# Kernel tuning notes

Measured on AMD Instinct MI355X. Metric: run time of the kernel, lower is better.

## Reference

```python
import math
import jax, jax.numpy as jnp
import numpy as np

HEADS = 16


def setup_inputs() -> dict:
    key = jax.random.key(0)
    k1, k2, k3, k4, k5 = jax.random.split(key, 5)
    B, S, D = 2, 2048, 1024
    return {
        "x": jax.random.normal(k1, (B, S, D), dtype=jnp.float32),
        "Wqkv": jax.random.normal(k2, (3 * D, D), dtype=jnp.float32) * (1.0 / math.sqrt(D)),
        "bqkv": jax.random.normal(k3, (3 * D,), dtype=jnp.float32) * 0.02,
        "Wo": jax.random.normal(k4, (D, D), dtype=jnp.float32) * (1.0 / math.sqrt(D)),
        "bo": jax.random.normal(k5, (D,), dtype=jnp.float32) * 0.02,
    }


def reference(x, Wqkv, bqkv, Wo, bo):
    B, S, D = x.shape
    H = HEADS
    hd = D // H  # head dim
    qkv = x @ Wqkv.T + bqkv                      # (B, S, 3D)
    # Faithful to torch: direct contiguous reshape (NOT a transpose-based head split)
    qkv = qkv.reshape(B, H, S, 3 * hd)           # (B, H, S, 3*hd)
    q, k, v = jnp.split(qkv, 3, axis=-1)         # each (B, H, S, hd)
    scores = jnp.einsum("bhsd,bhtd->bhst", q, k) * (1.0 / math.sqrt(hd))
    attn = jax.nn.softmax(scores, axis=-1)       # (B, H, S, S)
    vals = jnp.einsum("bhst,bhtd->bhsd", attn, v)
    vals = vals.reshape(B, S, D)                 # faithful direct reshape back
    return vals @ Wo.T + bo
```

## Files before the change

kernel.cpp:

```cpp
#include <hip/hip_runtime.h>
#include <stdint.h>

typedef unsigned short u16;
typedef __attribute__((ext_vector_type(8))) short short8;
typedef __attribute__((ext_vector_type(4))) float f32x4;
typedef __attribute__((ext_vector_type(16))) float f32x16;
typedef __attribute__((ext_vector_type(8))) __bf16 bf16x8;
typedef __attribute__((ext_vector_type(4))) unsigned u32x4;

#define DEV static __device__ __forceinline__

template <typename T>
DEV auto mfma_try(T a, T b, f32x4 c, int)
    -> decltype(__builtin_amdgcn_mfma_f32_16x16x32_bf16(a, b, c, 0, 0, 0)) {
  return __builtin_amdgcn_mfma_f32_16x16x32_bf16(a, b, c, 0, 0, 0);
}
template <typename T>
DEV f32x4 mfma_try(T a, T b, f32x4 c, long) {
  return __builtin_amdgcn_mfma_f32_16x16x32_bf16(
      __builtin_bit_cast(bf16x8, a), __builtin_bit_cast(bf16x8, b), c, 0, 0, 0);
}
DEV f32x4 MFMA(short8 a, short8 b, f32x4 c) { return mfma_try(a, b, c, 0); }

template <typename T>
DEV auto mfma32_try(T a, T b, f32x16 c, int)
    -> decltype(__builtin_amdgcn_mfma_f32_32x32x16_bf16(a, b, c, 0, 0, 0)) {
  return __builtin_amdgcn_mfma_f32_32x32x16_bf16(a, b, c, 0, 0, 0);
}
template <typename T>
DEV f32x16 mfma32_try(T a, T b, f32x16 c, long) {
  return __builtin_amdgcn_mfma_f32_32x32x16_bf16(
      __builtin_bit_cast(bf16x8, a), __builtin_bit_cast(bf16x8, b), c, 0, 0, 0);
}
DEV f32x16 MFMA32(short8 a, short8 b, f32x16 c) { return mfma32_try(a, b, c, 0); }

DEV void gload16(const u16* g, u16* lds) {
  __builtin_amdgcn_global_load_lds((unsigned int*)g, (unsigned int*)lds, 16, 0, 0);
}

DEV u16 f2bf(float f) {
  unsigned u = __float_as_uint(f);
  u = (u + 0x7FFFu + ((u >> 16) & 1u)) >> 16;
  return (u16)u;
}

DEV float exp2fast(float x) {
  float r;
  asm("v_exp_f32 %0, %1" : "=v"(r) : "v"(x));
  return r;
}

DEV unsigned cvtpk_bf16(float lo, float hi_) {
  unsigned r;
  asm("v_cvt_pk_bf16_f32 %0, %1, %2" : "=v"(r) : "v"(lo), "v"(hi_));
  return r;
}

DEV void permswap(unsigned& a, unsigned& b) {
  asm volatile("v_permlane32_swap_b32 %0, %1" : "+v"(a), "+v"(b));
}

__global__ void cvt_kernel(const float* __restrict__ x, const float* __restrict__ wq,
                           const float* __restrict__ wo, u16* __restrict__ xb,
                           u16* __restrict__ wqb, u16* __restrict__ wob) {
  const int N1 = 4194304 / 4, N2 = 3145728 / 4, N3 = 1048576 / 4;
  const int total = N1 + N2 + N3;
  for (int i = blockIdx.x * blockDim.x + threadIdx.x; i < total;
       i += gridDim.x * blockDim.x) {
    const float4* s;
    u16* d;
    int off;
    if (i < N1) { s = (const float4*)x; d = xb; off = i; }
    else if (i < N1 + N2) { s = (const float4*)wq; d = wqb; off = i - N1; }
    else { s = (const float4*)wo; d = wob; off = i - N1 - N2; }
    float4 v = s[off];
    ushort4 o;
    o.x = f2bf(v.x); o.y = f2bf(v.y); o.z = f2bf(v.z); o.w = f2bf(v.w);
    ((ushort4*)d)[off] = o;
  }
}

__global__ __launch_bounds__(256, 4) void gemm1_128(
    const u16* __restrict__ A, const u16* __restrict__ Bm,
    const float* __restrict__ bias,
    u16* __restrict__ Qb, u16* __restrict__ Kb, u16* __restrict__ Vb) {
  __shared__ u16 SM[128 * 136];
  u16* const As = SM;
  u16* const Bs = SM + 4096;
  const int K = 1024;
  const int tid = threadIdx.x;
  const int lane = tid & 63;
  const int wave = tid >> 6;
  const int wr = wave >> 1, wc = wave & 1;
  const int l15 = lane & 15, l4 = lane >> 4;
  const int m0 = blockIdx.y * 128, n0 = blockIdx.x * 128;

  f32x4 acc[4][4] = {};

  const u16* ga = A + (size_t)(m0 + (tid >> 2)) * K + (tid & 3) * 8;
  const u16* gb = Bm + (size_t)(n0 + (tid >> 2)) * K + (tid & 3) * 8;
  u16* la = As + tid * 8;
  u16* lb = Bs + tid * 8;
  const size_t rstep = (size_t)64 * K;

  for (int kt = 0; kt < K; kt += 32) {
    gload16(ga + kt, la);
    gload16(ga + kt + rstep, la + 2048);
    gload16(gb + kt, lb);
    gload16(gb + kt + rstep, lb + 2048);
    __syncthreads();
    short8 af[4], bfr[4];
#pragma unroll
    for (int i = 0; i < 4; ++i)
      af[i] = *(const short8*)(As + (wr * 64 + i * 16 + l15) * 32 + l4 * 8);
#pragma unroll
    for (int i = 0; i < 4; ++i)
      bfr[i] = *(const short8*)(Bs + (wc * 64 + i * 16 + l15) * 32 + l4 * 8);
#pragma unroll
    for (int i = 0; i < 4; ++i)
#pragma unroll
      for (int j = 0; j < 4; ++j) acc[i][j] = MFMA(af[i], bfr[j], acc[i][j]);
    __syncthreads();
  }

#pragma unroll
  for (int nj = 0; nj < 4; ++nj) {
    const int cl = wc * 64 + nj * 16 + l15;
    const float bv = bias[n0 + cl];
#pragma unroll
    for (int mi = 0; mi < 4; ++mi)
#pragma unroll
      for (int r = 0; r < 4; ++r) {
        const int ml = wr * 64 + mi * 16 + l4 * 4 + r;
        SM[ml * 136 + cl] = f2bf(acc[mi][nj][r] + bv);
      }
  }
  __syncthreads();

  const int ml = tid >> 1;
  const int h = tid & 1;
  const int m = m0 + ml;
  const int c0 = n0 + h * 64;
  const int chunk = c0 / 192;
  const int sel = (c0 - chunk * 192) >> 6;
  u16* const dst = (sel == 0) ? Qb : ((sel == 1) ? Kb : Vb);
  const int s = m & 2047;
  const int bh = (m >> 11) * 16 + (s >> 7);
  const int s2 = (s & 127) * 16 + chunk;
  u16* const drow = dst + ((size_t)bh * 2048 + s2) * 64;
  const u16* const srow = SM + ml * 136 + h * 64;
#pragma unroll
  for (int g = 0; g < 8; ++g)
    *(short8*)(drow + g * 8) = *(const short8*)(srow + g * 8);
}

__global__ __launch_bounds__(256, 4) void gemm2_64(
    const u16* __restrict__ A, const u16* __restrict__ Bm,
    const float* __restrict__ bias, float* __restrict__ Cf) {
  __shared__ u16 As[64 * 32];
  __shared__ u16 Bs[128 * 32];
  const int K = 1024, N = 1024;
  const int tid = threadIdx.x;
  const int lane = tid & 63;
  const int wave = tid >> 6;
  const int l15 = lane & 15, l4 = lane >> 4;
  const int m0 = blockIdx.y * 64, n0 = blockIdx.x * 128;

  f32x4 acc[4][2] = {};

  const u16* ga = A + (size_t)(m0 + (tid >> 2)) * K + (tid & 3) * 8;
  const u16* gb = Bm + (size_t)(n0 + (tid >> 2)) * K + (tid & 3) * 8;
  u16* la = As + tid * 8;
  u16* lb = Bs + tid * 8;
  const size_t rstep = (size_t)64 * K;

  for (int kt = 0; kt < K; kt += 32) {
    gload16(ga + kt, la);
    gload16(gb + kt, lb);
    gload16(gb + kt + rstep, lb + 2048);
    __syncthreads();
    short8 af[4], bfr[2];
#pragma unroll
    for (int i = 0; i < 4; ++i)
      af[i] = *(const short8*)(As + (i * 16 + l15) * 32 + l4 * 8);
#pragma unroll
    for (int j = 0; j < 2; ++j)
      bfr[j] = *(const short8*)(Bs + (wave * 32 + j * 16 + l15) * 32 + l4 * 8);
#pragma unroll
    for (int i = 0; i < 4; ++i)
#pragma unroll
      for (int j = 0; j < 2; ++j) acc[i][j] = MFMA(af[i], bfr[j], acc[i][j]);
    __syncthreads();
  }

#pragma unroll
  for (int nj = 0; nj < 2; ++nj) {
    const int c = n0 + wave * 32 + nj * 16 + l15;
    const float bv = bias[c];
#pragma unroll
    for (int mi = 0; mi < 4; ++mi)
#pragma unroll
      for (int r = 0; r < 4; ++r) {
        const int m = m0 + mi * 16 + l4 * 4 + r;
        Cf[(size_t)m * N + c] = acc[mi][nj][r] + bv;
      }
  }
}

__global__ __launch_bounds__(256) void vtrans_kernel(const u16* __restrict__ Vn,
                                                     u16* __restrict__ VT) {
  __shared__ u16 T[64 * 72];
  const int tid = threadIdx.x;
  const int bh = blockIdx.x >> 5;
  const int s0 = (blockIdx.x & 31) * 64;
  const int r = tid >> 3, c8 = tid & 7;
#pragma unroll
  for (int i = 0; i < 2; ++i) {
    const int s = r + i * 32;
    short8 v = *(const short8*)(Vn + ((size_t)bh * 2048 + s0 + s) * 64 + c8 * 8);
#pragma unroll
    for (int j = 0; j < 8; ++j) T[(c8 * 8 + j) * 72 + s] = (u16)v[j];
  }
  __syncthreads();
#pragma unroll
  for (int i = 0; i < 2; ++i) {
    const int d = (tid >> 3) + i * 32;
    short8 v = *(const short8*)(&T[d * 72 + (tid & 7) * 8]);
    *(short8*)(VT + ((size_t)bh * 64 + d) * 2048 + s0 + (tid & 7) * 8) = v;
  }
}

__global__ __launch_bounds__(512) void attn_kernel(
    const u16* __restrict__ Qg, const u16* __restrict__ Kg,
    const u16* __restrict__ VTg, u16* __restrict__ v2) {
  __shared__ __align__(16) char smem[65536];
  u16* const KS = (u16*)smem;
  u16* const VS = (u16*)smem + 16384;
  float* const FM = (float*)smem;

  const int tid = threadIdx.x;
  const int lane = tid & 63;
  const int half = tid >> 8;
  const int tid256 = tid & 255;
  const int w4 = (tid >> 6) & 3;
  const int l31 = lane & 31;
  const int hi = lane >> 5;

  const int bid = blockIdx.x;
  const int logical = (bid & 7) * 64 + (bid >> 3);
  const int bh = logical >> 4;
  const int qt = logical & 15;

  const u16* Qh = Qg + (size_t)bh * 2048 * 64;
  const u16* Kh = Kg + (size_t)bh * 2048 * 64;
  const u16* VTh = VTg + (size_t)bh * 64 * 2048;

  const int q0 = qt * 128 + w4 * 32;
  const float C1 = 0.18033688f;

  short8 qf[4];
#pragma unroll
  for (int d_ = 0; d_ < 4; ++d_)
    qf[d_] = *(const short8*)(Qh + (size_t)(q0 + l31) * 64 + d_ * 16 + hi * 8);

  f32x16 ot[2] = {};
  float ls4[4] = {0.f, 0.f, 0.f, 0.f};

  const int r8 = tid256 >> 3;
  const int c16 = tid256 & 7;
  const int xr = l31 & 7;
  const int Tbase = half * 16;

  auto stage = [&](int buf, int T) {
    u16* kd = KS + (half * 2 + buf) * 4096 + tid256 * 8;
    u16* vd = VS + (half * 2 + buf) * 4096 + tid256 * 8;
#pragma unroll
    for (int i = 0; i < 2; ++i) {
      const int row = i * 32 + r8;
      gload16(Kh + (size_t)(T * 64 + row) * 64 + ((c16 ^ (row & 7)) * 8),
              kd + i * 2048);
    }
#pragma unroll
    for (int i = 0; i < 2; ++i) {
      const int d = i * 32 + r8;
      gload16(VTh + (size_t)d * 2048 + T * 64 + ((c16 ^ (d & 7)) * 8),
              vd + i * 2048);
    }
  };

  stage(0, Tbase);
  __syncthreads();

  for (int t = 0; t < 16; ++t) {
    const int cur = t & 1;
    if (t + 1 < 16) stage(cur ^ 1, Tbase + t + 1);

    const u16* Kb = KS + (half * 2 + cur) * 4096;
    const u16* Vb = VS + (half * 2 + cur) * 4096;

    f32x16 st[2] = {};
    __builtin_amdgcn_s_setprio(1);
#pragma unroll
    for (int n = 0; n < 2; ++n)
#pragma unroll
      for (int d_ = 0; d_ < 4; ++d_) {
        short8 kf = *(const short8*)(Kb + (n * 32 + l31) * 64 +
                                     (((d_ * 2 + hi) ^ xr) * 8));
        st[n] = MFMA32(kf, qf[d_], st[n]);
      }
    __builtin_amdgcn_s_setprio(0);

#pragma unroll
    for (int r = 0; r < 16; ++r) {
      st[0][r] = exp2fast(st[0][r] * C1);
      st[1][r] = exp2fast(st[1][r] * C1);
    }
#pragma unroll
    for (int i = 0; i < 4; ++i)
      ls4[i] += ((st[0][i] + st[0][i + 4]) + (st[0][i + 8] + st[0][i + 12])) +
                ((st[1][i] + st[1][i + 4]) + (st[1][i + 8] + st[1][i + 12]));

    short8 pf[2][2];
#pragma unroll
    for (int n = 0; n < 2; ++n) {
      unsigned W[4][2];
#pragma unroll
      for (int j = 0; j < 4; ++j)
#pragma unroll
        for (int pp = 0; pp < 2; ++pp)
          W[j][pp] = cvtpk_bf16(st[n][4 * j + 2 * pp], st[n][4 * j + 2 * pp + 1]);
#pragma unroll
      for (int ks = 0; ks < 2; ++ks) {
        unsigned x0 = W[2 * ks][0], y0 = W[2 * ks + 1][0];
        unsigned x1 = W[2 * ks][1], y1 = W[2 * ks + 1][1];
        permswap(x0, y0);
        permswap(x1, y1);
        u32x4 pw = {x0, x1, y0, y1};
        pf[n][ks] = __builtin_bit_cast(short8, pw);
      }
    }

    __builtin_amdgcn_s_setprio(1);
#pragma unroll
    for (int db = 0; db < 2; ++db)
#pragma unroll
      for (int ksg = 0; ksg < 4; ++ksg) {
        short8 vf = *(const short8*)(Vb + (db * 32 + l31) * 64 +
                                     (((ksg * 2 + hi) ^ xr) * 8));
        ot[db] = MFMA32(vf, pf[ksg >> 1][ksg & 1], ot[db]);
      }
    __builtin_amdgcn_s_setprio(0);

    __syncthreads();
  }

  float l = (ls4[0] + ls4[1]) + (ls4[2] + ls4[3]);
  l += __shfl_xor(l, 32);

  if (half == 1) {
    float* F = FM + (size_t)(w4 * 64 + lane) * 33;
#pragma unroll
    for (int r = 0; r < 16; ++r) {
      F[r] = ot[0][r];
      F[16 + r] = ot[1][r];
    }
    F[32] = l;
  }
  __syncthreads();
  if (half == 0) {
    const float* F = FM + (size_t)(w4 * 64 + lane) * 33;
    const float inv = 1.0f / (l + F[32]);

    const int s2v = q0 + l31;
    const int rowO = (bh >> 4) * 2048 + (bh & 15) * 128 + (s2v >> 4);
    const int colb = (s2v & 15) * 64;
#pragma unroll
    for (int db = 0; db < 2; ++db)
#pragma unroll
      for (int g = 0; g < 4; ++g) {
        ushort4 w;
        w.x = f2bf((ot[db][4 * g + 0] + F[db * 16 + 4 * g + 0]) * inv);
        w.y = f2bf((ot[db][4 * g + 1] + F[db * 16 + 4 * g + 1]) * inv);
        w.z = f2bf((ot[db][4 * g + 2] + F[db * 16 + 4 * g + 2]) * inv);
        w.w = f2bf((ot[db][4 * g + 3] + F[db * 16 + 4 * g + 3]) * inv);
        const int d = db * 32 + 8 * g + 4 * hi;
        *(ushort4*)(v2 + (size_t)rowO * 1024 + colb + d) = w;
      }
  }
}

extern "C" void kernel_launch(void* const* d_in, const int* in_sizes, int n_in,
                              void* d_out, int out_size, void* d_ws, size_t ws_size,
                              hipStream_t stream) {
  const float* x = (const float*)d_in[0];
  const float* Wqkv = (const float*)d_in[1];
  const float* bqkv = (const float*)d_in[2];
  const float* Wo = (const float*)d_in[3];
  const float* bo = (const float*)d_in[4];
  float* out = (float*)d_out;

  char* ws = (char*)d_ws;
  u16* xb   = (u16*)(ws);
  u16* wqb  = (u16*)(ws + 8388608);
  u16* wob  = (u16*)(ws + 14680064);
  u16* Qb   = (u16*)(ws + 16777216);
  u16* Kb   = (u16*)(ws + 25165824);
  u16* VTb  = (u16*)(ws + 33554432);
  u16* v2   = (u16*)(ws + 41943040);
  u16* Vnat = v2;

  cvt_kernel<<<2048, 256, 0, stream>>>(x, Wqkv, Wo, xb, wqb, wob);

  dim3 g1(24, 32);
  gemm1_128<<<g1, 256, 0, stream>>>(xb, wqb, bqkv, Qb, Kb, Vnat);

  vtrans_kernel<<<1024, 256, 0, stream>>>(Vnat, VTb);

  attn_kernel<<<512, 512, 0, stream>>>(Qb, Kb, VTb, v2);

  dim3 g2(8, 64);
  gemm2_64<<<g2, 256, 0, stream>>>(v2, wob, bo, out);
}
```

Baseline: 118.8 us.

## Double-buffer LDS tiles in both projection GEMMs with async prefetch

```diff
diff --git a/kernel.cpp b/kernel.cpp
--- a/kernel.cpp
+++ b/kernel.cpp
@@ -85,8 +85,6 @@
     const float* __restrict__ bias,
     u16* __restrict__ Qb, u16* __restrict__ Kb, u16* __restrict__ Vb) {
   __shared__ u16 SM[128 * 136];
-  u16* const As = SM;
-  u16* const Bs = SM + 4096;
   const int K = 1024;
   const int tid = threadIdx.x;
   const int lane = tid & 63;
@@ -99,16 +97,30 @@
 
   const u16* ga = A + (size_t)(m0 + (tid >> 2)) * K + (tid & 3) * 8;
   const u16* gb = Bm + (size_t)(n0 + (tid >> 2)) * K + (tid & 3) * 8;
-  u16* la = As + tid * 8;
-  u16* lb = Bs + tid * 8;
   const size_t rstep = (size_t)64 * K;
 
-  for (int kt = 0; kt < K; kt += 32) {
+  auto stage = [&](int buf, int kt) {
+    u16* la = SM + buf * 8192 + tid * 8;
+    u16* lb = la + 4096;
     gload16(ga + kt, la);
     gload16(ga + kt + rstep, la + 2048);
     gload16(gb + kt, lb);
     gload16(gb + kt + rstep, lb + 2048);
-    __syncthreads();
+  };
+
+  stage(0, 0);
+  for (int t = 0; t < 32; ++t) {
+    const int cur = t & 1;
+    if (t + 1 < 32) {
+      stage(cur ^ 1, (t + 1) * 32);
+      asm volatile("s_waitcnt vmcnt(4)" ::: "memory");
+    } else {
+      asm volatile("s_waitcnt vmcnt(0)" ::: "memory");
+    }
+    __builtin_amdgcn_s_barrier();
+
+    const u16* As = SM + cur * 8192;
+    const u16* Bs = As + 4096;
     short8 af[4], bfr[4];
 #pragma unroll
     for (int i = 0; i < 4; ++i)
@@ -116,11 +128,13 @@
 #pragma unroll
     for (int i = 0; i < 4; ++i)
       bfr[i] = *(const short8*)(Bs + (wc * 64 + i * 16 + l15) * 32 + l4 * 8);
+    __builtin_amdgcn_s_setprio(1);
 #pragma unroll
     for (int i = 0; i < 4; ++i)
 #pragma unroll
       for (int j = 0; j < 4; ++j) acc[i][j] = MFMA(af[i], bfr[j], acc[i][j]);
-    __syncthreads();
+    __builtin_amdgcn_s_setprio(0);
+    __builtin_amdgcn_s_barrier();
   }
 
 #pragma unroll
@@ -157,8 +171,7 @@
 __global__ __launch_bounds__(256, 4) void gemm2_64(
     const u16* __restrict__ A, const u16* __restrict__ Bm,
     const float* __restrict__ bias, float* __restrict__ Cf) {
-  __shared__ u16 As[64 * 32];
-  __shared__ u16 Bs[128 * 32];
+  __shared__ u16 SM2[2 * 6144];
   const int K = 1024, N = 1024;
   const int tid = threadIdx.x;
   const int lane = tid & 63;
@@ -170,15 +183,29 @@
 
   const u16* ga = A + (size_t)(m0 + (tid >> 2)) * K + (tid & 3) * 8;
   const u16* gb = Bm + (size_t)(n0 + (tid >> 2)) * K + (tid & 3) * 8;
-  u16* la = As + tid * 8;
-  u16* lb = Bs + tid * 8;
   const size_t rstep = (size_t)64 * K;
 
-  for (int kt = 0; kt < K; kt += 32) {
+  auto stage = [&](int buf, int kt) {
+    u16* la = SM2 + buf * 6144 + tid * 8;
+    u16* lb = SM2 + buf * 6144 + 2048 + tid * 8;
     gload16(ga + kt, la);
     gload16(gb + kt, lb);
     gload16(gb + kt + rstep, lb + 2048);
-    __syncthreads();
+  };
+
+  stage(0, 0);
+  for (int t = 0; t < 32; ++t) {
+    const int cur = t & 1;
+    if (t + 1 < 32) {
+      stage(cur ^ 1, (t + 1) * 32);
+      asm volatile("s_waitcnt vmcnt(3)" ::: "memory");
+    } else {
+      asm volatile("s_waitcnt vmcnt(0)" ::: "memory");
+    }
+    __builtin_amdgcn_s_barrier();
+
+    const u16* As = SM2 + cur * 6144;
+    const u16* Bs = As + 2048;
     short8 af[4], bfr[2];
 #pragma unroll
     for (int i = 0; i < 4; ++i)
@@ -186,11 +213,13 @@
 #pragma unroll
     for (int j = 0; j < 2; ++j)
       bfr[j] = *(const short8*)(Bs + (wave * 32 + j * 16 + l15) * 32 + l4 * 8);
+    __builtin_amdgcn_s_setprio(1);
 #pragma unroll
     for (int i = 0; i < 4; ++i)
 #pragma unroll
       for (int j = 0; j < 2; ++j) acc[i][j] = MFMA(af[i], bfr[j], acc[i][j]);
-    __syncthreads();
+    __builtin_amdgcn_s_setprio(0);
+    __builtin_amdgcn_s_barrier();
   }
 
 #pragma unroll
```

Result: faster. 114.6 us (-3.5%).
